# Performance work log

Hardware: AMD Instinct MI355X
Metric: run time of the kernel (lower is better)

The kernel has to match this reference:

```python
import jax, jax.numpy as jnp
import numpy as np

E = 100000          # number of edges
NS, NV = 128, 64    # scalar / vector multiplicities of node irreps (128x0e + 64x1e)
FC = 64             # radial MLP width (fc_neurons = [64, 64])
WN = NS + NS + NV + NV + NV   # depthwise-TP weight numel = 448
VOUT = 64           # gated vector channels after linear
EPS = 1e-5
SQRT3 = 3.0 ** 0.5
SQRT2 = 2.0 ** 0.5


def setup_inputs() -> dict:
    key = jax.random.key(0)
    ks = jax.random.split(key, 12)

    def n(k, shape, scale=1.0):
        return jax.random.normal(k, shape, dtype=jnp.float32) * scale

    return dict(
        node_input=n(ks[0], (E, NS + 3 * NV)),   # [E, 320] gathered node features
        edge_attr=n(ks[1], (E, 4)),              # [E, 1(0e) + 3(1e)] spherical harmonics
        edge_scalars=n(ks[2], (E, FC)),          # [E, 64] radial embedding
        # radial MLP (RadialProfile): 64 -> 64 -> 64 -> 448 (+ offset)
        W1=n(ks[3], (FC, FC), FC ** -0.5), b1=jnp.zeros((FC,), jnp.float32),
        W2=n(ks[4], (FC, FC), FC ** -0.5), b2=jnp.zeros((FC,), jnp.float32),
        W3=n(ks[5], (FC, WN), FC ** -0.5), offset=jnp.zeros((WN,), jnp.float32),
        # irrep-wise linear (LinearRS): scalars 192->192 (incl. gates), vectors 256->64
        Ws=n(ks[6], (NS + NV, NS + NV), (NS + NV) ** -0.5),
        bs=jnp.zeros((NS + NV,), jnp.float32),
        Wv=n(ks[7], (NS + 2 * NV, VOUT), (NS + 2 * NV) ** -0.5),
        # equivariant layer-norm affine params
        g_s=jnp.ones((NS + NV,), jnp.float32), b_n=jnp.zeros((NS + NV,), jnp.float32),
        g_v=jnp.ones((VOUT,), jnp.float32),
    )


def _forward(node_input, edge_attr, edge_scalars, W1, b1, W2, b2, W3, offset,
             Ws, bs, Wv, g_s, b_n, g_v):
    # --- radial MLP -> per-edge depthwise-TP weights (dtp_rad) ---
    h = jax.nn.silu(edge_scalars @ W1 + b1)
    h = jax.nn.silu(h @ W2 + b2)
    w = h @ W3 + offset                                   # [E, 448]
    w1 = w[:, :NS]                 # 0e x 0e -> 0e  (128)
    w2 = w[:, NS:2 * NS]           # 0e x 1e -> 1e  (128)
    w3 = w[:, 2 * NS:2 * NS + NV]  # 1e x 0e -> 1e  (64)
    w4 = w[:, 2 * NS + NV:2 * NS + 2 * NV]   # 1e x 1e -> 0e (64)
    w5 = w[:, 2 * NS + 2 * NV:]              # 1e x 1e -> 1e (64)

    s = node_input[:, :NS]                    # [E, 128] scalar block
    v = node_input[:, NS:].reshape(-1, NV, 3) # [E, 64, 3] vector block
    e0 = edge_attr[:, 0:1]                    # [E, 1]
    e1 = edge_attr[:, 1:4]                    # [E, 3]

    # --- depthwise tensor product (per-edge CG contractions, 'uvu') ---
    o0a = w1 * s * e0                                          # [E,128]
    o0b = w4 * (v * e1[:, None, :]).sum(-1) / SQRT3            # [E,64]
    o1a = (w2 * s)[:, :, None] * e1[:, None, :]                # [E,128,3]
    o1b = w3[:, :, None] * v * e0[:, :, None]                  # [E,64,3]
    o1c = w5[:, :, None] * jnp.cross(v, e1[:, None, :]) / SQRT2  # [E,64,3]

    scal = jnp.concatenate([o0a, o0b], axis=-1)                # [E,192]
    vec = jnp.concatenate([o1a, o1b, o1c], axis=1)             # [E,256,3]

    # --- irrep-wise linear mix ---
    s_lin = scal @ Ws + bs                                     # [E,192]
    v_lin = jnp.einsum('euc,uo->eoc', vec, Wv)                 # [E,64,3]

    # --- equivariant layer norm (component normalization per irrep block) ---
    s_c = s_lin - s_lin.mean(-1, keepdims=True)
    s_norm = jax.lax.rsqrt((s_c ** 2).mean(-1, keepdims=True) + EPS)
    s_n = g_s * s_c * s_norm + b_n
    v_norm = jax.lax.rsqrt((v_lin ** 2).sum(-1).mean(-1) + EPS)  # [E]
    v_n = g_v[:, None] * v_lin * v_norm[:, None, None]

    # --- gated activation: SiLU on scalars, sigmoid gates on vectors ---
    out_s = jax.nn.silu(s_n[:, :NS])                           # [E,128]
    gates = jax.nn.sigmoid(s_n[:, NS:])                        # [E,64]
    out_v = v_n * gates[:, :, None]                            # [E,64,3]
    return jnp.concatenate([out_s, out_v.reshape(-1, 3 * VOUT)], axis=-1)


def reference(node_input, edge_attr, edge_scalars, W1, b1, W2, b2, W3, offset,
              Ws, bs, Wv, g_s, b_n, g_v):
    return _forward(node_input, edge_attr, edge_scalars, W1, b1, W2, b2, W3, offset,
                    Ws, bs, Wv, g_s, b_n, g_v)
```

## Files before the change

### kernel.cpp

```cpp
#include <hip/hip_runtime.h>

typedef short short8 __attribute__((ext_vector_type(8)));
typedef __bf16 bf16x8 __attribute__((ext_vector_type(8)));
typedef float f32x4 __attribute__((ext_vector_type(4)));

namespace {

constexpr int kNodeW = 320;
constexpr int kOutW  = 320;

constexpr int F_W1 = 0;
constexpr int F_W2 = 8;
constexpr int F_W3 = 16;
constexpr int F_WS = 72;
constexpr int F_WP = 144;
constexpr int F_WQ = 160;
constexpr int F_WR = 168;
constexpr int NFRAG = 176;

constexpr int WAVES = 4;
constexpr int ARENA_OFF = 128 * 1024;
constexpr int SMEM_SZ = 136 * 1024;

constexpr float RS3 = 0.5773502691896258f;
constexpr float RS2 = 0.7071067811865476f;

__device__ __forceinline__ ushort f2b(float f) {
  uint x = __float_as_uint(f);
  return (ushort)((x + 0x7FFFu + ((x >> 16) & 1u)) >> 16);
}
__device__ __forceinline__ float fsig(float x) { return 1.0f / (1.0f + __expf(-x)); }
__device__ __forceinline__ float fsilu(float x) { return x / (1.0f + __expf(-x)); }
__device__ __forceinline__ f32x4 MFMA(short8 a, short8 b, f32x4 c) {
  return __builtin_amdgcn_mfma_f32_16x16x32_bf16(
      __builtin_bit_cast(bf16x8, a), __builtin_bit_cast(bf16x8, b), c, 0, 0, 0);
}

__device__ __forceinline__ void cw16(char* ar, int row, int col, ushort v) {
  *(ushort*)(ar + ((row * 128 + col * 2) ^ ((row & 7) << 4))) = v;
}
__device__ __forceinline__ short8 cra(const char* ar, int row, int kb, int lg) {
  return *(const short8*)(ar + ((row * 128 + kb * 64 + lg * 16) ^ ((row & 7) << 4)));
}

__global__ void pack_weights(const float* __restrict__ W1, const float* __restrict__ W2,
                             const float* __restrict__ W3, const float* __restrict__ Ws,
                             const float* __restrict__ Wv, ushort* __restrict__ dst) {
  int f = blockIdx.x, lane = threadIdx.x;
  const float* src; int ldw, kbase, NT, local;
  if (f < 8)        { src = W1; ldw = 64;  kbase = 0;   NT = 4;  local = f; }
  else if (f < 16)  { src = W2; ldw = 64;  kbase = 0;   NT = 4;  local = f - 8; }
  else if (f < 72)  { src = W3; ldw = 448; kbase = 0;   NT = 28; local = f - 16; }
  else if (f < 144) { src = Ws; ldw = 192; kbase = 0;   NT = 12; local = f - 72; }
  else if (f < 160) { src = Wv; ldw = 64;  kbase = 0;   NT = 4;  local = f - 144; }
  else if (f < 168) { src = Wv; ldw = 64;  kbase = 128; NT = 4;  local = f - 160; }
  else              { src = Wv; ldw = 64;  kbase = 192; NT = 4;  local = f - 168; }
  int kb = local / NT, nt = local % NT;
  int k0  = kbase + kb * 32 + (lane >> 4) * 8;
  int col = nt * 16 + (lane & 15);
  ushort* o = dst + ((size_t)f * 64 + lane) * 8;
#pragma unroll
  for (int j = 0; j < 8; ++j) o[j] = f2b(src[(size_t)(k0 + j) * ldw + col]);
}

__global__ __launch_bounds__(256, 1) void fctp_main(
    const float* __restrict__ node, const float* __restrict__ eattr,
    const float* __restrict__ es, const float* __restrict__ b1,
    const float* __restrict__ b2, const float* __restrict__ offs,
    const float* __restrict__ bs, const float* __restrict__ g_s,
    const float* __restrict__ b_n, const float* __restrict__ g_v,
    const short8* __restrict__ wsv, float* __restrict__ out, int E) {
  __shared__ __align__(16) char smem[SMEM_SZ];
  const int lane = threadIdx.x & 63, wave = threadIdx.x >> 6;
  const int l15 = lane & 15, lg = lane >> 4;

#pragma unroll
  for (int i = 0; i < 32; ++i) {
    int fl = wave * 32 + i;
    int fg = (fl < 56) ? (F_W3 + fl) : (F_WS + (fl - 56));
    *(short8*)(smem + fl * 1024 + lane * 16) = wsv[fg * 64 + lane];
  }
  __syncthreads();

  char* ar = smem + ARENA_OFF + wave * 2048;
  auto ldsB = [&](int f) -> short8 {
    return *(const short8*)(smem + f * 1024 + lane * 16);
  };

  const int ntiles = (E + 15) >> 4;
  for (int tile = (int)blockIdx.x * WAVES + wave; tile < ntiles;
       tile += (int)gridDim.x * WAVES) {
    const int e0 = tile * 16;
    int geA = e0 + l15; if (geA >= E) geA = E - 1;
    int geR[4];
    float e0v[4], e1v[4][3];
#pragma unroll
    for (int r = 0; r < 4; ++r) {
      int g = e0 + lg * 4 + r; if (g >= E) g = E - 1;
      geR[r] = g;
      float4 ea = *(const float4*)(eattr + (size_t)g * 4);
      e0v[r] = ea.x; e1v[r][0] = ea.y; e1v[r][1] = ea.z; e1v[r][2] = ea.w;
    }

    float sn[4][8];
    float vn[4][4][3];
#pragma unroll
    for (int r = 0; r < 4; ++r) {
      const float* ni = node + (size_t)geR[r] * kNodeW;
#pragma unroll
      for (int nt = 0; nt < 8; ++nt) sn[r][nt] = ni[nt * 16 + l15];
#pragma unroll
      for (int nt = 0; nt < 4; ++nt) {
        const float* vp = ni + 128 + 3 * (nt * 16 + l15);
        vn[r][nt][0] = vp[0]; vn[r][nt][1] = vp[1]; vn[r][nt][2] = vp[2];
      }
    }

    short8 aes[2];
#pragma unroll
    for (int kb = 0; kb < 2; ++kb) {
      const float* p = es + (size_t)geA * 64 + kb * 32 + lg * 8;
      float4 xa = *(const float4*)p, xb = *(const float4*)(p + 4);
      short8 a;
      a[0] = (short)f2b(xa.x); a[1] = (short)f2b(xa.y); a[2] = (short)f2b(xa.z); a[3] = (short)f2b(xa.w);
      a[4] = (short)f2b(xb.x); a[5] = (short)f2b(xb.y); a[6] = (short)f2b(xb.z); a[7] = (short)f2b(xb.w);
      aes[kb] = a;
    }

    short8 ah[2];
    {
      f32x4 acc[4];
#pragma unroll
      for (int nt = 0; nt < 4; ++nt) { float bv = b1[nt * 16 + l15]; acc[nt] = (f32x4){bv, bv, bv, bv}; }
#pragma unroll
      for (int kb = 0; kb < 2; ++kb)
#pragma unroll
        for (int nt = 0; nt < 4; ++nt)
          acc[nt] = MFMA(aes[kb], wsv[(F_W1 + kb * 4 + nt) * 64 + lane], acc[nt]);
#pragma unroll
      for (int nt = 0; nt < 4; ++nt)
#pragma unroll
        for (int r = 0; r < 4; ++r)
          cw16(ar, lg * 4 + r, nt * 16 + l15, f2b(fsilu(acc[nt][r])));
      ah[0] = cra(ar, l15, 0, lg);
      ah[1] = cra(ar, l15, 1, lg);
    }
    {
      f32x4 acc[4];
#pragma unroll
      for (int nt = 0; nt < 4; ++nt) { float bv = b2[nt * 16 + l15]; acc[nt] = (f32x4){bv, bv, bv, bv}; }
#pragma unroll
      for (int kb = 0; kb < 2; ++kb)
#pragma unroll
        for (int nt = 0; nt < 4; ++nt)
          acc[nt] = MFMA(ah[kb], wsv[(F_W2 + kb * 4 + nt) * 64 + lane], acc[nt]);
#pragma unroll
      for (int nt = 0; nt < 4; ++nt)
#pragma unroll
        for (int r = 0; r < 4; ++r)
          cw16(ar, lg * 4 + r, nt * 16 + l15, f2b(fsilu(acc[nt][r])));
      ah[0] = cra(ar, l15, 0, lg);
      ah[1] = cra(ar, l15, 1, lg);
    }

    auto wseg = [&](int seg, f32x4 (&w)[4]) {
#pragma unroll
      for (int nt = 0; nt < 4; ++nt) {
        float bv = offs[seg * 64 + nt * 16 + l15];
        w[nt] = (f32x4){bv, bv, bv, bv};
      }
#pragma unroll
      for (int kb = 0; kb < 2; ++kb)
#pragma unroll
        for (int nt = 0; nt < 4; ++nt)
          w[nt] = MFMA(ah[kb], ldsB(kb * 28 + seg * 4 + nt), w[nt]);
    };
    auto gemm12 = [&](int kb0, f32x4 (&sac)[12]) {
      short8 a0 = cra(ar, l15, 0, lg), a1 = cra(ar, l15, 1, lg);
#pragma unroll
      for (int nt = 0; nt < 12; ++nt)
        sac[nt] = MFMA(a0, ldsB(56 + kb0 * 12 + nt), sac[nt]);
#pragma unroll
      for (int nt = 0; nt < 12; ++nt)
        sac[nt] = MFMA(a1, ldsB(56 + (kb0 + 1) * 12 + nt), sac[nt]);
    };
    auto gemm4 = [&](int fb0, int fb1, f32x4 (&ac)[4]) {
      short8 a0 = cra(ar, l15, 0, lg), a1 = cra(ar, l15, 1, lg);
#pragma unroll
      for (int nt = 0; nt < 4; ++nt) ac[nt] = MFMA(a0, wsv[(fb0 + nt) * 64 + lane], ac[nt]);
#pragma unroll
      for (int nt = 0; nt < 4; ++nt) ac[nt] = MFMA(a1, wsv[(fb1 + nt) * 64 + lane], ac[nt]);
    };
    auto tpS = [&](const f32x4 (&w)[4], int nb, bool mulE0) {
#pragma unroll
      for (int nt = 0; nt < 4; ++nt)
#pragma unroll
        for (int r = 0; r < 4; ++r) {
          float v = w[nt][r] * sn[r][nb + nt];
          if (mulE0) v *= e0v[r];
          cw16(ar, lg * 4 + r, nt * 16 + l15, f2b(v));
        }
    };
    auto tpD = [&](const f32x4 (&w)[4]) {
#pragma unroll
      for (int nt = 0; nt < 4; ++nt)
#pragma unroll
        for (int r = 0; r < 4; ++r) {
          float dot = vn[r][nt][0] * e1v[r][0] + vn[r][nt][1] * e1v[r][1] +
                      vn[r][nt][2] * e1v[r][2];
          cw16(ar, lg * 4 + r, nt * 16 + l15, f2b(w[nt][r] * dot * RS3));
        }
    };
    auto tpQ = [&](const f32x4 (&w)[4], int c) {
#pragma unroll
      for (int nt = 0; nt < 4; ++nt)
#pragma unroll
        for (int r = 0; r < 4; ++r)
          cw16(ar, lg * 4 + r, nt * 16 + l15, f2b(w[nt][r] * vn[r][nt][c]));
    };
    auto tpR = [&](const f32x4 (&w)[4], int c) {
      const int i1 = (c + 1) % 3, i2 = (c + 2) % 3;
#pragma unroll
      for (int nt = 0; nt < 4; ++nt)
#pragma unroll
        for (int r = 0; r < 4; ++r) {
          float cr = vn[r][nt][i1] * e1v[r][i2] - vn[r][nt][i2] * e1v[r][i1];
          cw16(ar, lg * 4 + r, nt * 16 + l15, f2b(w[nt][r] * cr * RS2));
        }
    };

    f32x4 wacc[4];
    f32x4 sacc[12];
#pragma unroll
    for (int nt = 0; nt < 12; ++nt) { float bv = bs[nt * 16 + l15]; sacc[nt] = (f32x4){bv, bv, bv, bv}; }
    wseg(0, wacc); tpS(wacc, 0, true);  gemm12(0, sacc);
    wseg(1, wacc); tpS(wacc, 4, true);  gemm12(2, sacc);
    wseg(5, wacc); tpD(wacc);           gemm12(4, sacc);

    float gate[4][4];
    {
      float gsv[12], bnv[12];
#pragma unroll
      for (int nt = 0; nt < 12; ++nt) { gsv[nt] = g_s[nt * 16 + l15]; bnv[nt] = b_n[nt * 16 + l15]; }
#pragma unroll
      for (int r = 0; r < 4; ++r) {
        float sx = 0.f, sxx = 0.f;
#pragma unroll
        for (int nt = 0; nt < 12; ++nt) { float v = sacc[nt][r]; sx += v; sxx += v * v; }
#pragma unroll
        for (int m = 8; m >= 1; m >>= 1) { sx += __shfl_xor(sx, m); sxx += __shfl_xor(sxx, m); }
        float mean = sx * (1.0f / 192.0f);
        float var  = sxx * (1.0f / 192.0f) - mean * mean;
        float rstd = rsqrtf(var + 1e-5f);
        int geu = e0 + lg * 4 + r;
        bool valid = geu < E;
        float* ob = out + (size_t)(valid ? geu : 0) * kOutW;
#pragma unroll
        for (int nt = 0; nt < 12; ++nt) {
          float s_n = gsv[nt] * (sacc[nt][r] - mean) * rstd + bnv[nt];
          if (nt < 8) { if (valid) ob[nt * 16 + l15] = fsilu(s_n); }
          else gate[r][nt - 8] = fsig(s_n);
        }
      }
    }

    f32x4 pacc[4];
#pragma unroll
    for (int nt = 0; nt < 4; ++nt) pacc[nt] = (f32x4){0.f, 0.f, 0.f, 0.f};
    wseg(2, wacc); tpS(wacc, 0, false); gemm4(F_WP,     F_WP + 4,  pacc);
    wseg(3, wacc); tpS(wacc, 4, false); gemm4(F_WP + 8, F_WP + 12, pacc);

    f32x4 vl[3][4];
    wseg(4, wacc);
#pragma unroll
    for (int c = 0; c < 3; ++c) {
      tpQ(wacc, c);
      f32x4 q[4];
#pragma unroll
      for (int nt = 0; nt < 4; ++nt) q[nt] = (f32x4){0.f, 0.f, 0.f, 0.f};
      gemm4(F_WQ, F_WQ + 4, q);
#pragma unroll
      for (int nt = 0; nt < 4; ++nt)
#pragma unroll
        for (int r = 0; r < 4; ++r)
          vl[c][nt][r] = pacc[nt][r] * e1v[r][c] + e0v[r] * q[nt][r];
    }
    wseg(6, wacc);
#pragma unroll
    for (int c = 0; c < 3; ++c) {
      tpR(wacc, c);
      gemm4(F_WR, F_WR + 4, vl[c]);
    }

    {
      float gvv[4];
#pragma unroll
      for (int nt = 0; nt < 4; ++nt) gvv[nt] = g_v[nt * 16 + l15];
#pragma unroll
      for (int r = 0; r < 4; ++r) {
        float vsq = 0.f;
#pragma unroll
        for (int c = 0; c < 3; ++c)
#pragma unroll
          for (int nt = 0; nt < 4; ++nt) { float v = vl[c][nt][r]; vsq += v * v; }
#pragma unroll
        for (int m = 8; m >= 1; m >>= 1) vsq += __shfl_xor(vsq, m);
        float vnrm = rsqrtf(vsq * (1.0f / 64.0f) + 1e-5f);
        int geu = e0 + lg * 4 + r;
        if (geu < E) {
          float* ob = out + (size_t)geu * kOutW + 128;
#pragma unroll
          for (int nt = 0; nt < 4; ++nt) {
            float m3 = gvv[nt] * vnrm * gate[r][nt];
            int o3 = (nt * 16 + l15) * 3;
            ob[o3 + 0] = m3 * vl[0][nt][r];
            ob[o3 + 1] = m3 * vl[1][nt][r];
            ob[o3 + 2] = m3 * vl[2][nt][r];
          }
        }
      }
    }
  }
}

}

extern "C" void kernel_launch(void* const* d_in, const int* in_sizes, int n_in,
                              void* d_out, int out_size, void* d_ws, size_t ws_size,
                              hipStream_t stream) {
  const float* node_input   = (const float*)d_in[0];
  const float* edge_attr    = (const float*)d_in[1];
  const float* edge_scalars = (const float*)d_in[2];
  const float* W1 = (const float*)d_in[3];
  const float* b1 = (const float*)d_in[4];
  const float* W2 = (const float*)d_in[5];
  const float* b2 = (const float*)d_in[6];
  const float* W3 = (const float*)d_in[7];
  const float* offset = (const float*)d_in[8];
  const float* Ws = (const float*)d_in[9];
  const float* bs = (const float*)d_in[10];
  const float* Wv = (const float*)d_in[11];
  const float* g_s = (const float*)d_in[12];
  const float* b_n = (const float*)d_in[13];
  const float* g_v = (const float*)d_in[14];
  float* out = (float*)d_out;

  const int E = in_sizes[0] / kNodeW;

  pack_weights<<<NFRAG, 64, 0, stream>>>(W1, W2, W3, Ws, Wv, (ushort*)d_ws);

  const int ntiles = (E + 15) / 16;
  int blocks = (ntiles + WAVES - 1) / WAVES;
  if (blocks > 256) blocks = 256;
  fctp_main<<<blocks, WAVES * 64, 0, stream>>>(
      node_input, edge_attr, edge_scalars, b1, b2, offset, bs, g_s, b_n, g_v,
      (const short8*)d_ws, out, E);
}
```

Baseline: 215.4 us.

## Triple-buffer LDS staging slots and batch TP GEMMs, moving Wq/Wr weights into LDS

Each wave now gets three staging slots in shared memory instead of one. All tensor-product operands for a stage are written first, then read back and fed to one batched run of MFMAs, so fewer write/read round trips serialize the GEMMs. The W3 segments 0-5 plus the Wq and Wr fragments are now cached in LDS, while segment 6 and Wp are read from global memory. The e0 factor is folded into the Q operand, so it is rounded to bf16 before the matmul. LDS use rises from 136KB to 160KB per block, and the extra register pressure from holding more A fragments is a risk.

```diff
diff --git a/kernel.cpp b/kernel.cpp
--- a/kernel.cpp
+++ b/kernel.cpp
@@ -19,8 +19,8 @@
 constexpr int NFRAG = 176;
 
 constexpr int WAVES = 4;
-constexpr int ARENA_OFF = 128 * 1024;
-constexpr int SMEM_SZ = 136 * 1024;
+constexpr int ARENA_OFF = 136 * 1024;
+constexpr int SMEM_SZ = 160 * 1024;
 
 constexpr float RS3 = 0.5773502691896258f;
 constexpr float RS2 = 0.7071067811865476f;
@@ -75,14 +75,19 @@
   const int l15 = lane & 15, lg = lane >> 4;
 
 #pragma unroll
-  for (int i = 0; i < 32; ++i) {
-    int fl = wave * 32 + i;
-    int fg = (fl < 56) ? (F_W3 + fl) : (F_WS + (fl - 56));
+  for (int i = 0; i < 34; ++i) {
+    int fl = wave * 34 + i;
+    int fg = (fl < 48)  ? (F_W3 + (fl / 24) * 28 + (fl % 24))
+           : (fl < 120) ? (F_WS + (fl - 48))
+           : (fl < 128) ? (F_WQ + (fl - 120))
+                        : (F_WR + (fl - 128));
     *(short8*)(smem + fl * 1024 + lane * 16) = wsv[fg * 64 + lane];
   }
   __syncthreads();
 
-  char* ar = smem + ARENA_OFF + wave * 2048;
+  char* s0 = smem + ARENA_OFF + wave * 6144;
+  char* s1 = s0 + 2048;
+  char* s2 = s0 + 4096;
   auto ldsB = [&](int f) -> short8 {
     return *(const short8*)(smem + f * 1024 + lane * 16);
   };
@@ -141,9 +146,9 @@
       for (int nt = 0; nt < 4; ++nt)
 #pragma unroll
         for (int r = 0; r < 4; ++r)
-          cw16(ar, lg * 4 + r, nt * 16 + l15, f2b(fsilu(acc[nt][r])));
-      ah[0] = cra(ar, l15, 0, lg);
-      ah[1] = cra(ar, l15, 1, lg);
+          cw16(s0, lg * 4 + r, nt * 16 + l15, f2b(fsilu(acc[nt][r])));
+      ah[0] = cra(s0, l15, 0, lg);
+      ah[1] = cra(s0, l15, 1, lg);
     }
     {
       f32x4 acc[4];
@@ -158,9 +163,9 @@
       for (int nt = 0; nt < 4; ++nt)
 #pragma unroll
         for (int r = 0; r < 4; ++r)
-          cw16(ar, lg * 4 + r, nt * 16 + l15, f2b(fsilu(acc[nt][r])));
-      ah[0] = cra(ar, l15, 0, lg);
-      ah[1] = cra(ar, l15, 1, lg);
+          cw16(s0, lg * 4 + r, nt * 16 + l15, f2b(fsilu(acc[nt][r])));
+      ah[0] = cra(s0, l15, 0, lg);
+      ah[1] = cra(s0, l15, 1, lg);
     }
 
     auto wseg = [&](int seg, f32x4 (&w)[4]) {
@@ -173,69 +178,100 @@
       for (int kb = 0; kb < 2; ++kb)
 #pragma unroll
         for (int nt = 0; nt < 4; ++nt)
-          w[nt] = MFMA(ah[kb], ldsB(kb * 28 + seg * 4 + nt), w[nt]);
-    };
-    auto gemm12 = [&](int kb0, f32x4 (&sac)[12]) {
-      short8 a0 = cra(ar, l15, 0, lg), a1 = cra(ar, l15, 1, lg);
-#pragma unroll
-      for (int nt = 0; nt < 12; ++nt)
-        sac[nt] = MFMA(a0, ldsB(56 + kb0 * 12 + nt), sac[nt]);
-#pragma unroll
-      for (int nt = 0; nt < 12; ++nt)
-        sac[nt] = MFMA(a1, ldsB(56 + (kb0 + 1) * 12 + nt), sac[nt]);
-    };
-    auto gemm4 = [&](int fb0, int fb1, f32x4 (&ac)[4]) {
-      short8 a0 = cra(ar, l15, 0, lg), a1 = cra(ar, l15, 1, lg);
-#pragma unroll
-      for (int nt = 0; nt < 4; ++nt) ac[nt] = MFMA(a0, wsv[(fb0 + nt) * 64 + lane], ac[nt]);
-#pragma unroll
-      for (int nt = 0; nt < 4; ++nt) ac[nt] = MFMA(a1, wsv[(fb1 + nt) * 64 + lane], ac[nt]);
-    };
-    auto tpS = [&](const f32x4 (&w)[4], int nb, bool mulE0) {
+          w[nt] = MFMA(ah[kb], ldsB(kb * 24 + seg * 4 + nt), w[nt]);
+    };
+    auto wseg6 = [&](f32x4 (&w)[4]) {
+#pragma unroll
+      for (int nt = 0; nt < 4; ++nt) {
+        float bv = offs[6 * 64 + nt * 16 + l15];
+        w[nt] = (f32x4){bv, bv, bv, bv};
+      }
+#pragma unroll
+      for (int kb = 0; kb < 2; ++kb)
+#pragma unroll
+        for (int nt = 0; nt < 4; ++nt)
+          w[nt] = MFMA(ah[kb], wsv[(F_W3 + kb * 28 + 24 + nt) * 64 + lane], w[nt]);
+    };
+    auto tpS = [&](char* slot, const f32x4 (&w)[4], int nb, bool mulE0) {
 #pragma unroll
       for (int nt = 0; nt < 4; ++nt)
 #pragma unroll
         for (int r = 0; r < 4; ++r) {
           float v = w[nt][r] * sn[r][nb + nt];
           if (mulE0) v *= e0v[r];
-          cw16(ar, lg * 4 + r, nt * 16 + l15, f2b(v));
+          cw16(slot, lg * 4 + r, nt * 16 + l15, f2b(v));
         }
     };
-    auto tpD = [&](const f32x4 (&w)[4]) {
+    auto tpD = [&](char* slot, const f32x4 (&w)[4]) {
 #pragma unroll
       for (int nt = 0; nt < 4; ++nt)
 #pragma unroll
         for (int r = 0; r < 4; ++r) {
           float dot = vn[r][nt][0] * e1v[r][0] + vn[r][nt][1] * e1v[r][1] +
                       vn[r][nt][2] * e1v[r][2];
-          cw16(ar, lg * 4 + r, nt * 16 + l15, f2b(w[nt][r] * dot * RS3));
+          cw16(slot, lg * 4 + r, nt * 16 + l15, f2b(w[nt][r] * dot * RS3));
         }
     };
-    auto tpQ = [&](const f32x4 (&w)[4], int c) {
+    auto tpQ = [&](char* slot, const f32x4 (&w)[4], int c) {
 #pragma unroll
       for (int nt = 0; nt < 4; ++nt)
 #pragma unroll
         for (int r = 0; r < 4; ++r)
-          cw16(ar, lg * 4 + r, nt * 16 + l15, f2b(w[nt][r] * vn[r][nt][c]));
-    };
-    auto tpR = [&](const f32x4 (&w)[4], int c) {
+          cw16(slot, lg * 4 + r, nt * 16 + l15,
+               f2b(e0v[r] * w[nt][r] * vn[r][nt][c]));
+    };
+    auto tpR = [&](char* slot, const f32x4 (&w)[4], int c) {
       const int i1 = (c + 1) % 3, i2 = (c + 2) % 3;
 #pragma unroll
       for (int nt = 0; nt < 4; ++nt)
 #pragma unroll
         for (int r = 0; r < 4; ++r) {
           float cr = vn[r][nt][i1] * e1v[r][i2] - vn[r][nt][i2] * e1v[r][i1];
-          cw16(ar, lg * 4 + r, nt * 16 + l15, f2b(w[nt][r] * cr * RS2));
+          cw16(slot, lg * 4 + r, nt * 16 + l15, f2b(w[nt][r] * cr * RS2));
         }
     };
 
-    f32x4 wacc[4];
     f32x4 sacc[12];
 #pragma unroll
     for (int nt = 0; nt < 12; ++nt) { float bv = bs[nt * 16 + l15]; sacc[nt] = (f32x4){bv, bv, bv, bv}; }
-    wseg(0, wacc); tpS(wacc, 0, true);  gemm12(0, sacc);
-    wseg(1, wacc); tpS(wacc, 4, true);  gemm12(2, sacc);
-    wseg(5, wacc); tpD(wacc);           gemm12(4, sacc);
+    {
+      f32x4 wa[4];
+      wseg(0, wa); tpS(s0, wa, 0, true);
+      wseg(1, wa); tpS(s1, wa, 4, true);
+      wseg(5, wa); tpD(s2, wa);
+      short8 sA[3][2];
+      sA[0][0] = cra(s0, l15, 0, lg); sA[0][1] = cra(s0, l15, 1, lg);
+      sA[1][0] = cra(s1, l15, 0, lg); sA[1][1] = cra(s1, l15, 1, lg);
+      sA[2][0] = cra(s2, l15, 0, lg); sA[2][1] = cra(s2, l15, 1, lg);
+#pragma unroll
+      for (int blk = 0; blk < 3; ++blk)
+#pragma unroll
+        for (int kb = 0; kb < 2; ++kb)
+#pragma unroll
+          for (int nt = 0; nt < 12; ++nt)
+            sacc[nt] = MFMA(sA[blk][kb], ldsB(48 + (blk * 2 + kb) * 12 + nt), sacc[nt]);
+    }
+
+    f32x4 pacc[4];
+#pragma unroll
+    for (int nt = 0; nt < 4; ++nt) pacc[nt] = (f32x4){0.f, 0.f, 0.f, 0.f};
+    {
+      f32x4 wa[4];
+      wseg(2, wa); tpS(s0, wa, 0, false);
+      wseg(3, wa); tpS(s1, wa, 4, false);
+      short8 pA[2][2];
+      pA[0][0] = cra(s0, l15, 0, lg); pA[0][1] = cra(s0, l15, 1, lg);
+      pA[1][0] = cra(s1, l15, 0, lg); pA[1][1] = cra(s1, l15, 1, lg);
+#pragma unroll
+      for (int blk = 0; blk < 2; ++blk)
+#pragma unroll
+        for (int kb = 0; kb < 2; ++kb)
+#pragma unroll
+          for (int nt = 0; nt < 4; ++nt)
+            pacc[nt] = MFMA(pA[blk][kb],
+                            wsv[(F_WP + (blk * 2 + kb) * 4 + nt) * 64 + lane],
+                            pacc[nt]);
+    }
 
     float gate[4][4];
     {
@@ -264,32 +300,45 @@
       }
     }
 
-    f32x4 pacc[4];
-#pragma unroll
-    for (int nt = 0; nt < 4; ++nt) pacc[nt] = (f32x4){0.f, 0.f, 0.f, 0.f};
-    wseg(2, wacc); tpS(wacc, 0, false); gemm4(F_WP,     F_WP + 4,  pacc);
-    wseg(3, wacc); tpS(wacc, 4, false); gemm4(F_WP + 8, F_WP + 12, pacc);
-
     f32x4 vl[3][4];
-    wseg(4, wacc);
-#pragma unroll
-    for (int c = 0; c < 3; ++c) {
-      tpQ(wacc, c);
-      f32x4 q[4];
-#pragma unroll
-      for (int nt = 0; nt < 4; ++nt) q[nt] = (f32x4){0.f, 0.f, 0.f, 0.f};
-      gemm4(F_WQ, F_WQ + 4, q);
-#pragma unroll
-      for (int nt = 0; nt < 4; ++nt)
-#pragma unroll
-        for (int r = 0; r < 4; ++r)
-          vl[c][nt][r] = pacc[nt][r] * e1v[r][c] + e0v[r] * q[nt][r];
-    }
-    wseg(6, wacc);
-#pragma unroll
-    for (int c = 0; c < 3; ++c) {
-      tpR(wacc, c);
-      gemm4(F_WR, F_WR + 4, vl[c]);
+    {
+      f32x4 wa[4];
+      wseg(4, wa);
+      tpQ(s0, wa, 0); tpQ(s1, wa, 1); tpQ(s2, wa, 2);
+#pragma unroll
+      for (int c = 0; c < 3; ++c)
+#pragma unroll
+        for (int nt = 0; nt < 4; ++nt)
+#pragma unroll
+          for (int r = 0; r < 4; ++r)
+            vl[c][nt][r] = pacc[nt][r] * e1v[r][c];
+      short8 qA[3][2];
+      qA[0][0] = cra(s0, l15, 0, lg); qA[0][1] = cra(s0, l15, 1, lg);
+      qA[1][0] = cra(s1, l15, 0, lg); qA[1][1] = cra(s1, l15, 1, lg);
+      qA[2][0] = cra(s2, l15, 0, lg); qA[2][1] = cra(s2, l15, 1, lg);
+#pragma unroll
+      for (int c = 0; c < 3; ++c)
+#pragma unroll
+        for (int kb = 0; kb < 2; ++kb)
+#pragma unroll
+          for (int nt = 0; nt < 4; ++nt)
+            vl[c][nt] = MFMA(qA[c][kb], ldsB(120 + kb * 4 + nt), vl[c][nt]);
+    }
+    {
+      f32x4 wa[4];
+      wseg6(wa);
+      tpR(s0, wa, 0); tpR(s1, wa, 1); tpR(s2, wa, 2);
+      short8 tA[3][2];
+      tA[0][0] = cra(s0, l15, 0, lg); tA[0][1] = cra(s0, l15, 1, lg);
+      tA[1][0] = cra(s1, l15, 0, lg); tA[1][1] = cra(s1, l15, 1, lg);
+      tA[2][0] = cra(s2, l15, 0, lg); tA[2][1] = cra(s2, l15, 1, lg);
+#pragma unroll
+      for (int c = 0; c < 3; ++c)
+#pragma unroll
+        for (int kb = 0; kb < 2; ++kb)
+#pragma unroll
+          for (int nt = 0; nt < 4; ++nt)
+            vl[c][nt] = MFMA(tA[c][kb], ldsB(128 + kb * 4 + nt), vl[c][nt]);
     }
 
     {
```

After: 230.2 us. 1.07x slower.
